# Kernel optimization log

Measured on AMD Instinct MI355X. Metric: run time of the kernel, lower is better.

## Reference

```python
import jax, jax.numpy as jnp
import numpy as np

K = 8            # top-k neighbors per channel
BN_EPS = 1e-3    # keras BatchNormalization default


def top_k_features(h, adj, k):
    # h: [N, F], adj: [N, N] (dense). Per node and per channel, take the k
    # largest masked neighbor feature values, then prepend the node's own feature.
    masked = adj[:, None, :] * h.T[None, :, :]        # [N, F, N]
    topk = jax.lax.top_k(masked, k)[0]                # [N, F, K]
    topk = jnp.transpose(topk, (0, 2, 1))             # [N, K, F]
    return jnp.concatenate([h[:, None, :], topk], axis=1)  # [N, K+1, F]


def conv1d(x, w):
    # x: [N, L, Cin], w: [kw, Cin, Cout], VALID 1D conv
    return jax.lax.conv_general_dilated(x, w, (1,), 'VALID',
                                        dimension_numbers=('NWC', 'WIO', 'NWC'))


def batchnorm(x, gamma, beta, mean, var):
    return gamma * (x - mean) * jax.lax.rsqrt(var + BN_EPS) + beta


def setup_inputs():
    key = jax.random.key(0)
    ks = jax.random.split(key, 16)
    N, Fin, H, Cout, NF = 1600, 1433, 32, 7, 8
    x = jax.random.normal(ks[0], (N, Fin), jnp.float32)
    # sparse binary adjacency, avg degree ~16
    adj = (jax.random.uniform(ks[1], (N, N)) < 0.01).astype(jnp.float32)
    mask = jax.random.uniform(ks[2], (N,)) < 0.5

    def g(k, shape, fan_in):
        return jax.random.normal(k, shape, jnp.float32) * (1.0 / np.sqrt(fan_in))

    W0 = g(ks[3], (Fin, H), Fin)                 # DenseConvolution (GCN) weight
    # LGConv block 1: F=32 -> mid (32+8)//2=20 -> 8; kernels 5,5 reduce 9->5->1
    W1a = g(ks[4], (5, 32, 20), 5 * 32)
    W1b = g(ks[5], (5, 20, NF), 5 * 20)
    # LGConv block 2: F=40 -> mid (40+8)//2=24 -> 8
    W2a = g(ks[6], (5, 40, 24), 5 * 40)
    W2b = g(ks[7], (5, 24, NF), 5 * 24)
    Wout = g(ks[8], (H + 2 * NF, Cout), H + 2 * NF)  # 48 -> 7
    bn = {}
    for i, kk in ((1, 9), (2, 12)):
        bn[f'g{i}'] = 1.0 + 0.1 * jax.random.normal(ks[kk], (NF,), jnp.float32)
        bn[f'b{i}'] = 0.1 * jax.random.normal(ks[kk + 1], (NF,), jnp.float32)
        bn[f'm{i}'] = 0.1 * jax.random.normal(ks[kk + 2], (NF,), jnp.float32)
        bn[f'v{i}'] = jax.random.uniform(ks[kk], (NF,), jnp.float32, 0.5, 1.5)
    return {'x': x, 'adj': adj, 'W0': W0, 'W1a': W1a, 'W1b': W1b,
            'W2a': W2a, 'W2b': W2b, 'Wout': Wout,
            'g1': bn['g1'], 'b1': bn['b1'], 'm1': bn['m1'], 'v1': bn['v1'],
            'g2': bn['g2'], 'b2': bn['b2'], 'm2': bn['m2'], 'v2': bn['v2'],
            'mask': mask}


def reference(x, adj, W0, W1a, W1b, W2a, W2b, Wout,
              g1, b1, m1, v1, g2, b2, m2, v2, mask):
    # inference mode: dropout = identity
    h = adj @ (x @ W0)                                # GCN layer, hidden=32
    for Wa, Wb, g, b, m, v in ((W1a, W1b, g1, b1, m1, v1),
                               (W2a, W2b, g2, b2, m2, v2)):
        t = top_k_features(h, adj, K)                 # [N, K+1, F]
        c = conv1d(t, Wa)                             # [N, 5, mid]
        c = conv1d(c, Wb)[:, 0, :]                    # [N, 8]
        c = batchnorm(c, g, b, m, v)
        h = jnp.concatenate([h, c], axis=-1)          # 32 -> 40 -> 48
    logits = adj @ (h @ Wout)                         # [N, 7]
    # Mask layer (boolean_mask); static-shape variant: zero out masked rows
    return jnp.where(mask[:, None], logits, 0.0)
```

## Files before the change

kernel.cpp:

```cpp
#include <hip/hip_runtime.h>


constexpr int NN   = 1600;
constexpr int FIN  = 1433;
constexpr int HGCN = 32;
constexpr int NBS  = 96;
constexpr float BN_EPS = 1e-3f;

constexpr int KS    = 16;
constexpr int CHUNK = 90;
constexpr int BM    = 32;
constexpr int SXS   = 92;
constexpr int RB    = NN / BM;
constexpr int CSRB  = 400;
constexpr int K1B   = CSRB + 1 + RB * KS;
constexpr int GB    = 256;
constexpr int NT    = 512;
constexpr int TS    = 44;
constexpr int ZBYTES = 225280;

__device__ __forceinline__ void astore(float* p, float v) {
    __hip_atomic_store(p, v, __ATOMIC_RELAXED, __HIP_MEMORY_SCOPE_AGENT);
}
__device__ __forceinline__ void astorei(int* p, int v) {
    __hip_atomic_store(p, v, __ATOMIC_RELAXED, __HIP_MEMORY_SCOPE_AGENT);
}
__device__ __forceinline__ int aloadi(const int* p) {
    return __hip_atomic_load(p, __ATOMIC_RELAXED, __HIP_MEMORY_SCOPE_AGENT);
}

__global__ __launch_bounds__(512) void zero_k(float4* __restrict__ p) {
    int i = blockIdx.x * 512 + threadIdx.x;
    if (i < ZBYTES / 16) p[i] = make_float4(0.f, 0.f, 0.f, 0.f);
}

__device__ __forceinline__ void gbar(int* cntrel, int phase) {
    int* cnt = cntrel + phase * GB;
    int* rel = cntrel + 896 + phase;
    __syncthreads();
    if (blockIdx.x == 0) {
        int s = threadIdx.x;
        if (s >= 1 && s < GB) {
            while (aloadi(&cnt[s]) == 0) __builtin_amdgcn_s_sleep(1);
        }
        __syncthreads();
        if (threadIdx.x == 0) astorei(rel, 1);
    } else {
        if (threadIdx.x == 0) {
            astorei(&cnt[blockIdx.x], 1);
            while (aloadi(rel) == 0) __builtin_amdgcn_s_sleep(1);
        }
    }
    __syncthreads();
}

__global__ __launch_bounds__(256) void k1(const float* __restrict__ x,
                                          const float* __restrict__ W0,
                                          const float* __restrict__ adj,
                                          const float* __restrict__ W1a,
                                          const float* __restrict__ W2a,
                                          int* __restrict__ deg,
                                          unsigned short* __restrict__ nbr,
                                          const unsigned char* __restrict__ mb,
                                          int* __restrict__ flag,
                                          float* __restrict__ wsT1,
                                          float* __restrict__ wsT2,
                                          float* __restrict__ h0) {
    __shared__ float sx[BM][SXS];
    __shared__ float sw[CHUNK * HGCN];
    int b = blockIdx.x, t = threadIdx.x;

    if (b < CSRB) {
        int lane = t & 63;
        int row  = b * 4 + (t >> 6);
        const float*  ar  = adj + (size_t)row * NN;
        const float4* ar4 = (const float4*)ar;
        unsigned short* nb = nbr + (size_t)row * NBS;
        int cnt = 0;
        #pragma unroll
        for (int it = 0; it < 6; ++it) {
            float4 v = ar4[it * 64 + lane];
            int base = it * 256 + 4 * lane;
            #pragma unroll
            for (int c = 0; c < 4; ++c) {
                float vc = (c == 0) ? v.x : (c == 1) ? v.y : (c == 2) ? v.z : v.w;
                bool p = (vc != 0.0f);
                unsigned long long m = __ballot(p);
                if (p) {
                    int off = cnt + __popcll(m & ((1ull << lane) - 1ull));
                    if (off < NBS) nb[off] = (unsigned short)(base + c);
                }
                cnt += __popcll(m);
            }
        }
        {
            float v = ar[1536 + lane];
            bool p = (v != 0.0f);
            unsigned long long m = __ballot(p);
            if (p) {
                int off = cnt + __popcll(m & ((1ull << lane) - 1ull));
                if (off < NBS) nb[off] = (unsigned short)(1536 + lane);
            }
            cnt += __popcll(m);
        }
        if (lane == 0) deg[row] = cnt < NBS ? cnt : NBS;
        return;
    }

    if (b == CSRB) {
        if (t < 64) {
            int lane = t;
            bool odd = false, flt = false;
            for (int i = lane; i < NN; i += 64) {
                unsigned char v = mb[i];
                if (v) {
                    int r = i & 3;
                    if (r != 0) odd = true;
                    if (r >= 2 && (v == 0x3F || v == 0x80)) flt = true;
                }
            }
            unsigned long long mo = __ballot(odd);
            unsigned long long mf = __ballot(flt);
            if (lane == 0) *flag = mf ? 2 : (mo ? 1 : 0);
        }
        for (int f = t; f < 800; f += 256) {
            int kw = f / 160, r = f - kw * 160, q = r / 20, o = r - q * 20;
            const float* wsrc = W1a + kw * 640 + 4 * q * 20 + o;
            float4 v;
            v.x = wsrc[0]; v.y = wsrc[20]; v.z = wsrc[40]; v.w = wsrc[60];
            ((float4*)wsT1)[f] = v;
        }
        for (int f = t; f < 1200; f += 256) {
            int kw = f / 240, r = f - kw * 240, q = r / 24, o = r - q * 24;
            const float* wsrc = W2a + kw * 960 + 4 * q * 24 + o;
            float4 v;
            v.x = wsrc[0]; v.y = wsrc[24]; v.z = wsrc[48]; v.w = wsrc[72];
            ((float4*)wsT2)[f] = v;
        }
        return;
    }

    int tile = b - (CSRB + 1);
    int rb   = tile % RB;
    int ks   = tile / RB;
    int lane = t & 31;
    int row0 = rb * BM;
    int k0   = ks * CHUNK;
    int vk   = FIN - k0; if (vk > CHUNK) vk = CHUNK;

    {
        int g = t >> 5;
        #pragma unroll
        for (int j = 0; j < 4; ++j) {
            int r = g + 8 * j;
            const float* xr = x + (size_t)(row0 + r) * FIN + k0;
            #pragma unroll
            for (int m = 0; m < 3; ++m) {
                int k = lane + 32 * m;
                if (k < CHUNK) sx[r][k] = (k < vk) ? xr[k] : 0.0f;
            }
        }
    }
    {
        const float4* w4  = (const float4*)(W0 + (size_t)k0 * HGCN);
        float4*       sw4 = (float4*)sw;
        int vf4 = vk * 8;
        for (int i = t; i < CHUNK * 8; i += 256)
            sw4[i] = (i < vf4) ? w4[i] : make_float4(0.f, 0.f, 0.f, 0.f);
    }
    __syncthreads();

    int col = lane;
    int rq  = t >> 5;
    float acc0 = 0.f, acc1 = 0.f, acc2 = 0.f, acc3 = 0.f;
    #pragma unroll 4
    for (int kk = 0; kk < 88; kk += 4) {
        float4 a0 = *(const float4*)&sx[rq     ][kk];
        float4 a1 = *(const float4*)&sx[rq +  8][kk];
        float4 a2 = *(const float4*)&sx[rq + 16][kk];
        float4 a3 = *(const float4*)&sx[rq + 24][kk];
        float w0v = sw[(kk + 0) * HGCN + col];
        float w1v = sw[(kk + 1) * HGCN + col];
        float w2v = sw[(kk + 2) * HGCN + col];
        float w3v = sw[(kk + 3) * HGCN + col];
        acc0 += a0.x * w0v + a0.y * w1v + a0.z * w2v + a0.w * w3v;
        acc1 += a1.x * w0v + a1.y * w1v + a1.z * w2v + a1.w * w3v;
        acc2 += a2.x * w0v + a2.y * w1v + a2.z * w2v + a2.w * w3v;
        acc3 += a3.x * w0v + a3.y * w1v + a3.z * w2v + a3.w * w3v;
    }
    #pragma unroll
    for (int kk = 88; kk < CHUNK; ++kk) {
        float wv = sw[kk * HGCN + col];
        acc0 += sx[rq     ][kk] * wv;
        acc1 += sx[rq +  8][kk] * wv;
        acc2 += sx[rq + 16][kk] * wv;
        acc3 += sx[rq + 24][kk] * wv;
    }

    atomicAdd(&h0[(row0 + rq     ) * HGCN + col], acc0);
    atomicAdd(&h0[(row0 + rq +  8) * HGCN + col], acc1);
    atomicAdd(&h0[(row0 + rq + 16) * HGCN + col], acc2);
    atomicAdd(&h0[(row0 + rq + 24) * HGCN + col], acc3);
}

template<int F, int MID, bool WRITEZ>
__device__ __forceinline__ void lgconv_phase(int b, int wave, int lane,
        const int* __restrict__ deg, const unsigned short* __restrict__ nbr,
        const float* sWt, const float* sWb,
        const float* __restrict__ g, const float* __restrict__ bb,
        const float* __restrict__ mm, const float* __restrict__ vv,
        const float* __restrict__ h32, const float* __restrict__ c1in,
        const float* __restrict__ Wout,
        float* __restrict__ outbuf, float* T, float* C1) {
    int row = b + 256 * wave;
    if (row >= NN) return;
    int d = deg[row];
    const unsigned short* nb = nbr + (size_t)row * NBS;

    bool tk = (F == 32) ? (lane < 32) : (lane >= 32 && lane < 40);
    if (tk) {
        float t0=0.f,t1=0.f,t2=0.f,t3=0.f,t4=0.f,t5=0.f,t6=0.f,t7=0.f;
        #define BUBBLE(val_) { float val=val_, c;                       \
            c = t0; t0 = fmaxf(c, val); val = fminf(c, val);            \
            c = t1; t1 = fmaxf(c, val); val = fminf(c, val);            \
            c = t2; t2 = fmaxf(c, val); val = fminf(c, val);            \
            c = t3; t3 = fmaxf(c, val); val = fminf(c, val);            \
            c = t4; t4 = fmaxf(c, val); val = fminf(c, val);            \
            c = t5; t5 = fmaxf(c, val); val = fminf(c, val);            \
            c = t6; t6 = fmaxf(c, val); val = fminf(c, val);            \
            c = t7; t7 = fmaxf(c, val); val = fminf(c, val); }
        #define LDV(n_) ((F == 32) ? h32[(n_) * HGCN + lane]            \
                                   : c1in[(n_) * 8 + (lane - 32)])
        int it = 0;
        for (; it + 8 <= d; it += 8) {
            float v[8];
            #pragma unroll
            for (int j = 0; j < 8; ++j) v[j] = LDV((int)nb[it + j]);
            #pragma unroll
            for (int j = 0; j < 8; ++j) BUBBLE(v[j]);
        }
        for (; it < d; ++it) BUBBLE(LDV((int)nb[it]));
        T[0*TS+lane] = LDV(row);
        T[1*TS+lane] = t0; T[2*TS+lane] = t1; T[3*TS+lane] = t2; T[4*TS+lane] = t3;
        T[5*TS+lane] = t4; T[6*TS+lane] = t5; T[7*TS+lane] = t6; T[8*TS+lane] = t7;
        #undef LDV
        #undef BUBBLE
    }

    if (lane < MID) {
        int o = lane;
        float4 a0 = {0,0,0,0}, a1 = {0,0,0,0}, a2 = {0,0,0,0},
               a3 = {0,0,0,0}, a4 = {0,0,0,0};
        for (int q = 0; q < F / 4; ++q) {
            float4 tq[9];
            #pragma unroll
            for (int pos = 0; pos < 9; ++pos)
                tq[pos] = *(const float4*)&T[pos * TS + 4 * q];
            #pragma unroll
            for (int kw = 0; kw < 5; ++kw) {
                float4 wv = ((const float4*)sWt)[(kw * (F / 4) + q) * MID + o];
                #define ACC(ap_, pos_) { float4 tv = tq[pos_];          \
                    ap_.x += tv.x * wv.x; ap_.y += tv.y * wv.y;         \
                    ap_.z += tv.z * wv.z; ap_.w += tv.w * wv.w; }
                ACC(a0, kw + 0) ACC(a1, kw + 1) ACC(a2, kw + 2)
                ACC(a3, kw + 3) ACC(a4, kw + 4)
                #undef ACC
            }
        }
        C1[0 * MID + o] = (a0.x + a0.y) + (a0.z + a0.w);
        C1[1 * MID + o] = (a1.x + a1.y) + (a1.z + a1.w);
        C1[2 * MID + o] = (a2.x + a2.y) + (a2.z + a2.w);
        C1[3 * MID + o] = (a3.x + a3.y) + (a3.z + a3.w);
        C1[4 * MID + o] = (a4.x + a4.y) + (a4.z + a4.w);
    }

    {
        int grp = lane >> 3, o = lane & 7;
        float acc = 0.f;
        for (int idx = grp; idx < 5 * MID; idx += 8)
            acc += C1[idx] * sWb[idx * 8 + o];
        acc += __shfl_xor(acc, 8);
        acc += __shfl_xor(acc, 16);
        acc += __shfl_xor(acc, 32);
        float y = g[o] * (acc - mm[o]) * rsqrtf(vv[o] + BN_EPS) + bb[o];

        if (!WRITEZ) {
            if (lane < 8) astore(&outbuf[row * 8 + lane], y);
        } else {
            float yv[8];
            #pragma unroll
            for (int j = 0; j < 8; ++j) yv[j] = __shfl(y, j);
            if (lane < 8) {
                float z = 0.f;
                if (lane < 7) {
                    const float4* tf = (const float4*)T;
                    #pragma unroll
                    for (int k4 = 0; k4 < 10; ++k4) {
                        float4 tv = tf[k4];
                        z += tv.x * Wout[(4 * k4 + 0) * 7 + lane]
                           + tv.y * Wout[(4 * k4 + 1) * 7 + lane]
                           + tv.z * Wout[(4 * k4 + 2) * 7 + lane]
                           + tv.w * Wout[(4 * k4 + 3) * 7 + lane];
                    }
                    #pragma unroll
                    for (int j = 0; j < 8; ++j)
                        z += yv[j] * Wout[(40 + j) * 7 + lane];
                }
                astore(&outbuf[row * 8 + lane], z);
            }
        }
    }
}

__global__ __launch_bounds__(NT) void k2(
        const int* __restrict__ deg, const unsigned short* __restrict__ nbr,
        const float* __restrict__ h0,
        float* __restrict__ h32, float* __restrict__ c1, float* __restrict__ zbuf,
        const float* __restrict__ wsT1, const float* __restrict__ wsT2,
        const float* __restrict__ W1b,
        const float* __restrict__ g1, const float* __restrict__ b1,
        const float* __restrict__ m1, const float* __restrict__ v1,
        const float* __restrict__ W2b,
        const float* __restrict__ g2, const float* __restrict__ b2,
        const float* __restrict__ m2, const float* __restrict__ v2,
        const float* __restrict__ Wout, const void* __restrict__ mask,
        const int* __restrict__ flag, int* __restrict__ cntrel,
        float* __restrict__ out) {
    __shared__ float sWt1[3200];
    __shared__ float sWt2[4800];
    __shared__ float sWb1[800];
    __shared__ float sWb2[960];
    __shared__ float T   [8][9 * TS + 4];
    __shared__ float C1s [8][120];
    int t = threadIdx.x, b = blockIdx.x;
    int wave = t >> 6, lane = t & 63;

    {
        const float4* s1 = (const float4*)wsT1;
        const float4* s2 = (const float4*)wsT2;
        const float4* s3 = (const float4*)W1b;
        const float4* s4 = (const float4*)W2b;
        float4* d1 = (float4*)sWt1;
        float4* d2 = (float4*)sWt2;
        float4* d3 = (float4*)sWb1;
        float4* d4 = (float4*)sWb2;
        for (int i = t; i < 800;  i += NT) d1[i] = s1[i];
        for (int i = t; i < 1200; i += NT) d2[i] = s2[i];
        for (int i = t; i < 200;  i += NT) d3[i] = s3[i];
        for (int i = t; i < 240;  i += NT) d4[i] = s4[i];
    }

    {
        int row = b + 256 * wave;
        if (row < NN) {
            int f = lane & 31, half = lane >> 5;
            int d = deg[row];
            const unsigned short* nb = nbr + (size_t)row * NBS;
            float acc = 0.f;
            int it = half;
            for (; it + 16 <= d; it += 16) {
                float v[8];
                #pragma unroll
                for (int j = 0; j < 8; ++j) v[j] = h0[(int)nb[it + 2 * j] * HGCN + f];
                #pragma unroll
                for (int j = 0; j < 8; ++j) acc += v[j];
            }
            for (; it < d; it += 2) acc += h0[(int)nb[it] * HGCN + f];
            acc += __shfl_xor(acc, 32);
            if (half == 0) astore(&h32[row * HGCN + f], acc);
        }
    }
    gbar(cntrel, 0);

    lgconv_phase<32, 20, false>(b, wave, lane, deg, nbr, sWt1, sWb1,
                                g1, b1, m1, v1, h32, nullptr, Wout, c1,
                                T[wave], C1s[wave]);
    gbar(cntrel, 1);

    lgconv_phase<40, 24, true>(b, wave, lane, deg, nbr, sWt2, sWb2,
                               g2, b2, m2, v2, h32, c1, Wout, zbuf,
                               T[wave], C1s[wave]);
    gbar(cntrel, 2);

    {
        int row = b + 256 * wave;
        if (row < NN) {
            int d = deg[row];
            const unsigned short* nb = nbr + (size_t)row * NBS;
            int ng = lane >> 3, c = lane & 7;
            float acc = 0.f;
            for (int it = ng; it < d; it += 8)
                acc += zbuf[(int)nb[it] * 8 + c];
            acc += __shfl_xor(acc, 8);
            acc += __shfl_xor(acc, 16);
            acc += __shfl_xor(acc, 32);
            if (lane < 7) {
                int fl = *flag;
                bool mk;
                if (fl == 2)      mk = ((const float*)mask)[row] != 0.0f;
                else if (fl == 1) mk = ((const unsigned char*)mask)[row] != 0;
                else              mk = ((const int*)mask)[row] != 0;
                out[row * 7 + lane] = mk ? acc : 0.0f;
            }
        }
    }
}

extern "C" void kernel_launch(void* const* d_in, const int* in_sizes, int n_in,
                              void* d_out, int out_size, void* d_ws, size_t ws_size,
                              hipStream_t stream) {
    const float* x    = (const float*)d_in[0];
    const float* adj  = (const float*)d_in[1];
    const float* W0   = (const float*)d_in[2];
    const float* W1a  = (const float*)d_in[3];
    const float* W1b  = (const float*)d_in[4];
    const float* W2a  = (const float*)d_in[5];
    const float* W2b  = (const float*)d_in[6];
    const float* Wout = (const float*)d_in[7];
    const float* g1 = (const float*)d_in[8];
    const float* b1 = (const float*)d_in[9];
    const float* m1 = (const float*)d_in[10];
    const float* v1 = (const float*)d_in[11];
    const float* g2 = (const float*)d_in[12];
    const float* b2 = (const float*)d_in[13];
    const float* m2 = (const float*)d_in[14];
    const float* v2 = (const float*)d_in[15];
    const void*  mask = d_in[16];

    char* ws = (char*)d_ws;
    int*            cntrel = (int*)(ws + 0);
    float*          h0     = (float*)(ws + 20480);
    int*            flag   = (int*)(ws + 225280);
    int*            deg    = (int*)(ws + 225792);
    unsigned short* nbr    = (unsigned short*)(ws + 232192);
    float*          h32    = (float*)(ws + 539392);
    float*          c1     = (float*)(ws + 744192);
    float*          zbuf   = (float*)(ws + 795392);
    float*          wsT1   = (float*)(ws + 846592);
    float*          wsT2   = (float*)(ws + 859392);

    float* out = (float*)d_out;

    zero_k<<<(ZBYTES / 16 + 511) / 512, 512, 0, stream>>>((float4*)ws);
    k1<<<K1B, 256, 0, stream>>>(x, W0, adj, W1a, W2a, deg, nbr,
                                (const unsigned char*)mask, flag, wsT1, wsT2, h0);
    k2<<<GB, NT, 0, stream>>>(deg, nbr, h0, h32, c1, zbuf, wsT1, wsT2,
                              W1b, g1, b1, m1, v1,
                              W2b, g2, b2, m2, v2,
                              Wout, mask, flag, cntrel, out);
}
```

Before: 48.42 us.

## Replace atomic split-K accumulation with partial buffers and drop zeroing kernel

The GEMM split-K blocks now write partial sums to per-split buffers instead of doing atomicAdd into a zeroed h0, and the first phase of the persistent kernel reduces the 16 partials before a new grid barrier. This removes the separate zeroing launch, since the barrier counters are now cleared inside k1. The release flag is also spread over 32 padded slots to reduce polling contention. The cost is an extra grid barrier and extra global traffic to write and read the partials.

```diff
diff --git a/kernel.cpp b/kernel.cpp
--- a/kernel.cpp
+++ b/kernel.cpp
@@ -17,7 +17,6 @@
 constexpr int GB    = 256;
 constexpr int NT    = 512;
 constexpr int TS    = 44;
-constexpr int ZBYTES = 225280;
 
 __device__ __forceinline__ void astore(float* p, float v) {
     __hip_atomic_store(p, v, __ATOMIC_RELAXED, __HIP_MEMORY_SCOPE_AGENT);
@@ -29,14 +28,8 @@
     return __hip_atomic_load(p, __ATOMIC_RELAXED, __HIP_MEMORY_SCOPE_AGENT);
 }
 
-__global__ __launch_bounds__(512) void zero_k(float4* __restrict__ p) {
-    int i = blockIdx.x * 512 + threadIdx.x;
-    if (i < ZBYTES / 16) p[i] = make_float4(0.f, 0.f, 0.f, 0.f);
-}
-
 __device__ __forceinline__ void gbar(int* cntrel, int phase) {
     int* cnt = cntrel + phase * GB;
-    int* rel = cntrel + 896 + phase;
     __syncthreads();
     if (blockIdx.x == 0) {
         int s = threadIdx.x;
@@ -44,11 +37,13 @@
             while (aloadi(&cnt[s]) == 0) __builtin_amdgcn_s_sleep(1);
         }
         __syncthreads();
-        if (threadIdx.x == 0) astorei(rel, 1);
+        if (threadIdx.x < 32)
+            astorei(&cntrel[1024 + threadIdx.x * 32 + phase], 1);
     } else {
         if (threadIdx.x == 0) {
             astorei(&cnt[blockIdx.x], 1);
-            while (aloadi(rel) == 0) __builtin_amdgcn_s_sleep(1);
+            while (aloadi(&cntrel[1024 + (blockIdx.x & 31) * 32 + phase]) == 0)
+                __builtin_amdgcn_s_sleep(1);
         }
     }
     __syncthreads();
@@ -65,7 +60,8 @@
                                           int* __restrict__ flag,
                                           float* __restrict__ wsT1,
                                           float* __restrict__ wsT2,
-                                          float* __restrict__ h0) {
+                                          int* __restrict__ cntrel,
+                                          float* __restrict__ hp) {
     __shared__ float sx[BM][SXS];
     __shared__ float sw[CHUNK * HGCN];
     int b = blockIdx.x, t = threadIdx.x;
@@ -108,6 +104,7 @@
     }
 
     if (b == CSRB) {
+        for (int i = t; i < 2048; i += 256) cntrel[i] = 0;
         if (t < 64) {
             int lane = t;
             bool odd = false, flt = false;
@@ -197,10 +194,11 @@
         acc3 += sx[rq + 24][kk] * wv;
     }
 
-    atomicAdd(&h0[(row0 + rq     ) * HGCN + col], acc0);
-    atomicAdd(&h0[(row0 + rq +  8) * HGCN + col], acc1);
-    atomicAdd(&h0[(row0 + rq + 16) * HGCN + col], acc2);
-    atomicAdd(&h0[(row0 + rq + 24) * HGCN + col], acc3);
+    float* o = hp + (size_t)ks * NN * HGCN + (size_t)(row0 + rq) * HGCN + col;
+    o[0 * 8 * HGCN] = acc0;
+    o[1 * 8 * HGCN] = acc1;
+    o[2 * 8 * HGCN] = acc2;
+    o[3 * 8 * HGCN] = acc3;
 }
 
 template<int F, int MID, bool WRITEZ>
@@ -314,7 +312,7 @@
 
 __global__ __launch_bounds__(NT) void k2(
         const int* __restrict__ deg, const unsigned short* __restrict__ nbr,
-        const float* __restrict__ h0,
+        const float* __restrict__ hp, float* __restrict__ h0,
         float* __restrict__ h32, float* __restrict__ c1, float* __restrict__ zbuf,
         const float* __restrict__ wsT1, const float* __restrict__ wsT2,
         const float* __restrict__ W1b,
@@ -351,6 +349,17 @@
     }
 
     {
+        if (t < 200) {
+            int e = b * 200 + t;
+            float s = 0.f;
+            #pragma unroll
+            for (int ks = 0; ks < KS; ++ks) s += hp[(size_t)ks * NN * HGCN + e];
+            astore(&h0[e], s);
+        }
+    }
+    gbar(cntrel, 0);
+
+    {
         int row = b + 256 * wave;
         if (row < NN) {
             int f = lane & 31, half = lane >> 5;
@@ -370,17 +379,17 @@
             if (half == 0) astore(&h32[row * HGCN + f], acc);
         }
     }
-    gbar(cntrel, 0);
+    gbar(cntrel, 1);
 
     lgconv_phase<32, 20, false>(b, wave, lane, deg, nbr, sWt1, sWb1,
                                 g1, b1, m1, v1, h32, nullptr, Wout, c1,
                                 T[wave], C1s[wave]);
-    gbar(cntrel, 1);
+    gbar(cntrel, 2);
 
     lgconv_phase<40, 24, true>(b, wave, lane, deg, nbr, sWt2, sWb2,
                                g2, b2, m2, v2, h32, c1, Wout, zbuf,
                                T[wave], C1s[wave]);
-    gbar(cntrel, 2);
+    gbar(cntrel, 3);
 
     {
         int row = b + 256 * wave;
@@ -429,22 +438,23 @@
 
     char* ws = (char*)d_ws;
     int*            cntrel = (int*)(ws + 0);
-    float*          h0     = (float*)(ws + 20480);
-    int*            flag   = (int*)(ws + 225280);
-    int*            deg    = (int*)(ws + 225792);
-    unsigned short* nbr    = (unsigned short*)(ws + 232192);
-    float*          h32    = (float*)(ws + 539392);
-    float*          c1     = (float*)(ws + 744192);
-    float*          zbuf   = (float*)(ws + 795392);
-    float*          wsT1   = (float*)(ws + 846592);
-    float*          wsT2   = (float*)(ws + 859392);
+    int*            flag   = (int*)(ws + 8192);
+    int*            deg    = (int*)(ws + 8704);
+    unsigned short* nbr    = (unsigned short*)(ws + 16384);
+    float*          h0     = (float*)(ws + 323584);
+    float*          h32    = (float*)(ws + 528384);
+    float*          c1     = (float*)(ws + 733184);
+    float*          zbuf   = (float*)(ws + 784384);
+    float*          wsT1   = (float*)(ws + 835584);
+    float*          wsT2   = (float*)(ws + 848384);
+    float*          hp     = (float*)(ws + 868352);
 
     float* out = (float*)d_out;
 
-    zero_k<<<(ZBYTES / 16 + 511) / 512, 512, 0, stream>>>((float4*)ws);
     k1<<<K1B, 256, 0, stream>>>(x, W0, adj, W1a, W2a, deg, nbr,
-                                (const unsigned char*)mask, flag, wsT1, wsT2, h0);
-    k2<<<GB, NT, 0, stream>>>(deg, nbr, h0, h32, c1, zbuf, wsT1, wsT2,
+                                (const unsigned char*)mask, flag,
+                                wsT1, wsT2, cntrel, hp);
+    k2<<<GB, NT, 0, stream>>>(deg, nbr, hp, h0, h32, c1, zbuf, wsT1, wsT2,
                               W1b, g1, b1, m1, v1,
                               W2b, g2, b2, m2, v2,
                               Wout, mask, flag, cntrel, out);
```

Result: faster. 45.82 us (median of 2 runs) (-5.4%).
